# Kernel tuning notes

Measured on AMD Instinct MI355X. Metric: run time of the kernel, lower is better.

Reference implementation:

```python
import jax, jax.numpy as jnp
import numpy as np

EPS = 1e-5
NUM_HEADS = 8


def setup_inputs() -> dict:
    key = jax.random.key(0)
    ks = jax.random.split(key, 6)
    B, C, S = 4, 512, 2048
    std = 0.02
    return {
        "hidden_states": jax.random.normal(ks[0], (B, C, S), dtype=jnp.float32),
        "gn_weight": jnp.ones((C,), dtype=jnp.float32),
        "gn_bias": jnp.zeros((C,), dtype=jnp.float32),
        "wq": jax.random.normal(ks[1], (C, C), dtype=jnp.float32) * std,
        "bq": jnp.zeros((C,), dtype=jnp.float32),
        "wk": jax.random.normal(ks[2], (C, C), dtype=jnp.float32) * std,
        "bk": jnp.zeros((C,), dtype=jnp.float32),
        "wv": jax.random.normal(ks[3], (C, C), dtype=jnp.float32) * std,
        "bv": jnp.zeros((C,), dtype=jnp.float32),
        "wo": jax.random.normal(ks[4], (C, C), dtype=jnp.float32) * std,
        "bo": jnp.zeros((C,), dtype=jnp.float32),
    }


def reference(hidden_states, gn_weight, gn_bias, wq, bq, wk, bk, wv, bv, wo, bo):
    # hidden_states: [B, C, S]
    x = hidden_states
    B, C, S = x.shape
    H = NUM_HEADS
    D = C // H

    # GroupNorm with 1 group: normalize over (C, S) per sample
    mean = jnp.mean(x, axis=(1, 2), keepdims=True)
    var = jnp.var(x, axis=(1, 2), keepdims=True)
    h = (x - mean) * jax.lax.rsqrt(var + EPS)
    h = h * gn_weight[None, :, None] + gn_bias[None, :, None]

    h = jnp.swapaxes(h, 1, 2)  # [B, S, C]

    q = h @ wq.T + bq  # [B, S, C]
    k = h @ wk.T + bk
    v = h @ wv.T + bv

    # split heads: [B, H, S, D]
    q = q.reshape(B, S, H, D).transpose(0, 2, 1, 3)
    k = k.reshape(B, S, H, D).transpose(0, 2, 1, 3)
    v = v.reshape(B, S, H, D).transpose(0, 2, 1, 3)

    scale = 1.0 / (D ** 0.25)  # applied to both q and k, as in source
    scores = jnp.einsum('bhqd,bhkd->bhqk', q * scale, k * scale)
    probs = jax.nn.softmax(scores, axis=-1)
    out = jnp.einsum('bhqk,bhkd->bhqd', probs, v)  # [B, H, S, D]

    out = out.transpose(0, 2, 1, 3).reshape(B, S, C)  # [B, S, C]
    out = out @ wo.T + bo
    out = jnp.swapaxes(out, 1, 2)  # [B, C, S]
    return out + hidden_states
```

## Files before the change

### kernel.cpp

```cpp
#include <hip/hip_runtime.h>

typedef __attribute__((ext_vector_type(8))) __bf16 bf16x8;
typedef __attribute__((ext_vector_type(4))) __bf16 bf16x4;
typedef __attribute__((ext_vector_type(4))) float f32x4;
typedef __attribute__((ext_vector_type(16))) float f32x16;

#define BSZ 4
#define CCH 512
#define SEQ 2048
#define NH  8
#define HD  64

__device__ __forceinline__ f32x4 mfma16(bf16x8 a, bf16x8 b, f32x4 c) {
  return __builtin_amdgcn_mfma_f32_16x16x32_bf16(a, b, c, 0, 0, 0);
}
__device__ __forceinline__ f32x16 mfma32(bf16x8 a, bf16x8 b, f32x16 c) {
  return __builtin_amdgcn_mfma_f32_32x32x16_bf16(a, b, c, 0, 0, 0);
}

__device__ __forceinline__ void gload16(const void* g, void* l) {
  __builtin_amdgcn_global_load_lds((const __attribute__((address_space(1))) void*)g,
                                   (__attribute__((address_space(3))) void*)l,
                                   16, 0, 0);
}

__device__ __forceinline__ unsigned cvtpk(float lo, float hi) {
  unsigned r;
  asm("v_cvt_pk_bf16_f32 %0, %1, %2" : "=v"(r) : "v"(lo), "v"(hi));
  return r;
}
__device__ __forceinline__ void pl32swap(unsigned& a, unsigned& b) {
  asm("v_permlane32_swap_b32 %0, %1" : "+v"(a), "+v"(b));
}

__global__ __launch_bounds__(256) void gn_partial(const float* __restrict__ x,
                                                  float* __restrict__ stats) {
  int b = blockIdx.y;
  const float4* xb = (const float4*)(x + ((size_t)b << 20) + (size_t)blockIdx.x * 16384);
  int tid = threadIdx.x;
  float s = 0.f, sq = 0.f;
#pragma unroll
  for (int i = 0; i < 16; ++i) {
    float4 v = xb[i * 256 + tid];
    s  += v.x + v.y + v.z + v.w;
    sq += v.x * v.x + v.y * v.y + v.z * v.z + v.w * v.w;
  }
#pragma unroll
  for (int o = 32; o > 0; o >>= 1) { s += __shfl_down(s, o); sq += __shfl_down(sq, o); }
  __shared__ float ls[4], lq[4];
  int w = tid >> 6;
  if ((tid & 63) == 0) { ls[w] = s; lq[w] = sq; }
  __syncthreads();
  if (tid == 0) {
    float S = ls[0] + ls[1] + ls[2] + ls[3];
    float Q = lq[0] + lq[1] + lq[2] + lq[3];
    atomicAdd(&stats[b], S);
    atomicAdd(&stats[4 + b], Q);
  }
}

__global__ void gn_final(float* stats) {
  int t = threadIdx.x;
  if (t < 4) {
    const float n = 1048576.f;
    float mean = stats[t] / n;
    float var = stats[4 + t] / n - mean * mean;
    stats[8 + t]  = mean;
    stats[12 + t] = rsqrtf(var + 1e-5f);
  }
}

__global__ __launch_bounds__(256) void norm_tr(const float* __restrict__ x,
                                               const float* __restrict__ gw,
                                               const float* __restrict__ gb,
                                               const float* __restrict__ stats,
                                               __bf16* __restrict__ h) {
  int s0 = blockIdx.x * 64, c0 = blockIdx.y * 64, b = blockIdx.z;
  float mean = stats[8 + b], rstd = stats[12 + b];
  const float* xb = x + ((size_t)b << 20);
  __shared__ __align__(16) __bf16 tile[64][72];
  int tid = threadIdx.x;
#pragma unroll
  for (int j = 0; j < 16; ++j) {
    int e = tid + j * 256;
    int cl = e >> 6, sl = e & 63;
    float vv = xb[(size_t)(c0 + cl) * 2048 + s0 + sl];
    float hn = (vv - mean) * rstd * gw[c0 + cl] + gb[c0 + cl];
    tile[cl][sl] = (__bf16)hn;
  }
  __syncthreads();
#pragma unroll
  for (int j = 0; j < 2; ++j) {
    int row = (tid >> 3) + j * 32;
    int cg = tid & 7;
    bf16x8 pk;
#pragma unroll
    for (int e = 0; e < 8; ++e) pk[e] = tile[cg * 8 + e][row];
    *(bf16x8*)&h[(size_t)((b << 11) + s0 + row) * 512 + c0 + cg * 8] = pk;
  }
}

__global__ __launch_bounds__(256) void wcvt(const float* __restrict__ wq, const float* __restrict__ wk,
                                            const float* __restrict__ wv, const float* __restrict__ wo,
                                            __bf16* __restrict__ out) {
  int i = blockIdx.x * 256 + threadIdx.x;
  out[i]          = (__bf16)wq[i];
  out[262144 + i] = (__bf16)wk[i];
  out[524288 + i] = (__bf16)wv[i];
  out[786432 + i] = (__bf16)wo[i];
}

__global__ __launch_bounds__(256) void gemm_qkv(const __bf16* __restrict__ A, const __bf16* __restrict__ Wb,
                                                const float* __restrict__ bq, const float* __restrict__ bk,
                                                const float* __restrict__ bvv,
                                                __bf16* __restrict__ oq, __bf16* __restrict__ ok,
                                                __bf16* __restrict__ ov) {
  __shared__ __align__(16) __bf16 As[128 * 64];
  __shared__ __align__(16) __bf16 Bs[128 * 64];
  int z = blockIdx.z;
  const __bf16* W = Wb + (size_t)z * 262144;
  const float* bias = z == 0 ? bq : (z == 1 ? bk : bvv);
  __bf16* out = z == 0 ? oq : (z == 1 ? ok : ov);
  int tid = threadIdx.x, wid = tid >> 6, l = tid & 63;
  int m0 = blockIdx.x * 128, n0 = blockIdx.y * 128;
  int wm = (wid >> 1) * 64, wn = (wid & 1) * 64;
  int l16 = l & 15, lg = l >> 4;
  f32x4 zero = {0.f, 0.f, 0.f, 0.f};
  f32x4 acc[4][4];
#pragma unroll
  for (int mt = 0; mt < 4; ++mt)
#pragma unroll
    for (int nt = 0; nt < 4; ++nt) acc[mt][nt] = zero;
  int srow = wid * 32 + (l >> 3);
  int scol = (l & 7) * 8;
  for (int k0 = 0; k0 < 512; k0 += 64) {
    __syncthreads();
#pragma unroll
    for (int t = 0; t < 4; ++t) {
      gload16(A + (size_t)(m0 + srow + t * 8) * 512 + k0 + scol, &As[(wid * 32 + t * 8) * 64]);
      gload16(W + (size_t)(n0 + srow + t * 8) * 512 + k0 + scol, &Bs[(wid * 32 + t * 8) * 64]);
    }
    __syncthreads();
#pragma unroll
    for (int kk = 0; kk < 64; kk += 32) {
      bf16x8 af[4], bfr[4];
#pragma unroll
      for (int mt = 0; mt < 4; ++mt) af[mt] = *(const bf16x8*)&As[(wm + mt * 16 + l16) * 64 + kk + lg * 8];
#pragma unroll
      for (int nt = 0; nt < 4; ++nt) bfr[nt] = *(const bf16x8*)&Bs[(wn + nt * 16 + l16) * 64 + kk + lg * 8];
#pragma unroll
      for (int mt = 0; mt < 4; ++mt)
#pragma unroll
        for (int nt = 0; nt < 4; ++nt) acc[mt][nt] = mfma16(af[mt], bfr[nt], acc[mt][nt]);
    }
  }
#pragma unroll
  for (int nt = 0; nt < 4; ++nt) {
    int col = n0 + wn + nt * 16 + l16;
    float bb = bias[col];
#pragma unroll
    for (int mt = 0; mt < 4; ++mt)
#pragma unroll
      for (int r = 0; r < 4; ++r)
        out[(size_t)(m0 + wm + mt * 16 + lg * 4 + r) * 512 + col] = (__bf16)(acc[mt][nt][r] + bb);
  }
}

__global__ __launch_bounds__(256) void v_tr(const __bf16* __restrict__ v, __bf16* __restrict__ vt) {
  int s0 = blockIdx.x * 64, hh = blockIdx.y, b = blockIdx.z;
  __shared__ __align__(16) __bf16 tile[64][72];
  int tid = threadIdx.x;
#pragma unroll
  for (int j = 0; j < 16; ++j) {
    int e = tid + j * 256;
    int sl = e >> 6, dl = e & 63;
    tile[dl][sl] = v[(size_t)((b << 11) + s0 + sl) * 512 + hh * 64 + dl];
  }
  __syncthreads();
  const size_t base = (size_t)((b * 8 + hh) * 64) * 2048;
#pragma unroll
  for (int j = 0; j < 2; ++j) {
    int d = tid >> 2;
    int ch = (tid & 3) + j * 4;
    bf16x8 pk = *(const bf16x8*)&tile[d][ch * 8];
    *(bf16x8*)&vt[base + (size_t)d * 2048 + s0 + ch * 8] = pk;
  }
}

__global__ __launch_bounds__(256) void attn(const __bf16* __restrict__ q, const __bf16* __restrict__ k,
                                            const __bf16* __restrict__ vt, __bf16* __restrict__ ao) {
  const float C2 = 0.18033688011f;
  const float THR = 8.0f;
  int tid = threadIdx.x, w = tid >> 6, l = tid & 63;
  int q0w = blockIdx.x * 128 + w * 32;
  int hh = blockIdx.y, b = blockIdx.z;
  int l31 = l & 31, hi = l >> 5;

  __shared__ __align__(16) __bf16 smem[2][8192];

  bf16x8 qf[4];
  {
    const __bf16* qrow = q + ((size_t)((b << 11) + q0w + l31)) * 512 + hh * 64 + hi * 8;
#pragma unroll
    for (int dt = 0; dt < 4; ++dt) qf[dt] = *(const bf16x8*)&qrow[dt * 16];
  }

  const __bf16* kbase = k + ((size_t)(b << 11)) * 512 + hh * 64;
  const __bf16* vtb = vt + ((size_t)((b * 8 + hh) * 64)) * 2048;

  f32x16 zero16 = {};
  f32x16 o2[2];
  o2[0] = zero16; o2[1] = zero16;
  float m_run = -3.0e38f, l_run = 0.f;

  int rloc = l >> 3;
  int slotg = (l & 7) ^ rloc;
  int swz = (l31 & 7);

  auto STAGE = [&](int buf, int kv0) {
#pragma unroll
    for (int i = 0; i < 4; ++i) {
      int c = w * 4 + i;
      int row = (c & 7) * 8 + rloc;
      if (c < 8) {
        gload16(kbase + (size_t)(kv0 + row) * 512 + slotg * 8, &smem[buf][c * 512]);
      } else {
        gload16(vtb + (size_t)row * 2048 + kv0 + slotg * 8, &smem[buf][4096 + (c - 8) * 512]);
      }
    }
  };

  auto COMPUTE = [&](int buf) {
    const __bf16* Kt = &smem[buf][0];
    const __bf16* Vts = &smem[buf][4096];
    f32x16 sc[2];
#pragma unroll
    for (int kb = 0; kb < 2; ++kb) {
      sc[kb] = zero16;
      int r = kb * 32 + l31;
      __builtin_amdgcn_s_setprio(1);
#pragma unroll
      for (int dt = 0; dt < 4; ++dt) {
        bf16x8 kf = *(const bf16x8*)&Kt[r * 64 + ((dt * 2 + hi) ^ swz) * 8];
        sc[kb] = mfma32(kf, qf[dt], sc[kb]);
      }
      __builtin_amdgcn_s_setprio(0);
    }

    float mx01 = -3.0e38f;
#pragma unroll
    for (int kb = 0; kb < 2; ++kb)
#pragma unroll
      for (int r = 0; r < 16; ++r) mx01 = fmaxf(mx01, sc[kb][r]);
    mx01 = fmaxf(mx01, __shfl_xor(mx01, 32));
    mx01 *= C2;
    if (!__all(mx01 <= m_run + THR)) {
      float mnew = fmaxf(m_run, mx01);
      float alpha = exp2f(m_run - mnew);
      m_run = mnew;
      l_run *= alpha;
#pragma unroll
      for (int dblk = 0; dblk < 2; ++dblk)
#pragma unroll
        for (int r = 0; r < 16; ++r) o2[dblk][r] *= alpha;
    }
    float rs = 0.f;
#pragma unroll
    for (int kb = 0; kb < 2; ++kb)
#pragma unroll
      for (int r = 0; r < 16; ++r) {
        float p = exp2f(__builtin_fmaf(sc[kb][r], C2, -m_run));
        rs += p;
        sc[kb][r] = p;
      }
    rs += __shfl_xor(rs, 32);
    l_run += rs;

#pragma unroll
    for (int t = 0; t < 4; ++t) {
      int kb = t >> 1, h8 = (t & 1) * 8;
      unsigned u0 = cvtpk(sc[kb][h8 + 0], sc[kb][h8 + 1]);
      unsigned u1 = cvtpk(sc[kb][h8 + 2], sc[kb][h8 + 3]);
      unsigned u2 = cvtpk(sc[kb][h8 + 4], sc[kb][h8 + 5]);
      unsigned u3 = cvtpk(sc[kb][h8 + 6], sc[kb][h8 + 7]);
      pl32swap(u0, u2);
      pl32swap(u1, u3);
      union { unsigned u[4]; bf16x8 v; } pb;
      pb.u[0] = u0; pb.u[1] = u1; pb.u[2] = u2; pb.u[3] = u3;
      __builtin_amdgcn_s_setprio(1);
#pragma unroll
      for (int dblk = 0; dblk < 2; ++dblk) {
        int r = dblk * 32 + l31;
        bf16x8 vf = *(const bf16x8*)&Vts[r * 64 + ((t * 2 + hi) ^ swz) * 8];
        o2[dblk] = mfma32(vf, pb.v, o2[dblk]);
      }
      __builtin_amdgcn_s_setprio(0);
    }
  };

  int cur = 0;
  STAGE(0, 0);
  __syncthreads();
  for (int t = 0; t < 32; ++t) {
    if (t + 1 < 32) STAGE(cur ^ 1, (t + 1) * 64);
    COMPUTE(cur);
    __syncthreads();
    cur ^= 1;
  }

  float invl = 1.0f / l_run;
  __bf16* T = &smem[0][w * 2048];
  int swzq = (l31 & 7) * 8;
#pragma unroll
  for (int dblk = 0; dblk < 2; ++dblk)
#pragma unroll
    for (int g = 0; g < 4; ++g) {
      unsigned w0 = cvtpk(o2[dblk][g * 4 + 0] * invl, o2[dblk][g * 4 + 1] * invl);
      unsigned w1 = cvtpk(o2[dblk][g * 4 + 2] * invl, o2[dblk][g * 4 + 3] * invl);
      int d4 = dblk * 32 + g * 8 + hi * 4;
      uint2 pk2; pk2.x = w0; pk2.y = w1;
      *(uint2*)&T[l31 * 64 + (d4 ^ swzq)] = pk2;
    }
  int qr = l >> 1, hf = l & 1;
  int swzr = (qr & 7) * 8;
  __bf16* aorow = ao + (size_t)((b << 11) + q0w + qr) * 512 + hh * 64;
#pragma unroll
  for (int m = 0; m < 2; ++m) {
    int e = hf * 32 + m * 16;
    bf16x8 v0 = *(const bf16x8*)&T[qr * 64 + ((e) ^ swzr)];
    bf16x8 v1 = *(const bf16x8*)&T[qr * 64 + ((e + 8) ^ swzr)];
    *(bf16x8*)&aorow[e] = v0;
    *(bf16x8*)&aorow[e + 8] = v1;
  }
}

__global__ __launch_bounds__(256) void gemm_proj(const __bf16* __restrict__ A, const __bf16* __restrict__ W,
                                                 const float* __restrict__ bias,
                                                 const float* __restrict__ resid,
                                                 float* __restrict__ outp) {
  __shared__ __align__(16) union UU {
    struct SS { __bf16 a[128 * 64]; __bf16 b[128 * 64]; } s;
    float st[128 * 129];
  } u;
  int tid = threadIdx.x, wid = tid >> 6, l = tid & 63;
  int m0 = blockIdx.x * 128, n0 = blockIdx.y * 128;
  int wm = (wid >> 1) * 64, wn = (wid & 1) * 64;
  int l16 = l & 15, lg = l >> 4;
  f32x4 zero = {0.f, 0.f, 0.f, 0.f};
  f32x4 acc[4][4];
#pragma unroll
  for (int mt = 0; mt < 4; ++mt)
#pragma unroll
    for (int nt = 0; nt < 4; ++nt) acc[mt][nt] = zero;
  int srow = wid * 32 + (l >> 3);
  int scol = (l & 7) * 8;
  for (int k0 = 0; k0 < 512; k0 += 64) {
    __syncthreads();
#pragma unroll
    for (int t = 0; t < 4; ++t) {
      gload16(A + (size_t)(m0 + srow + t * 8) * 512 + k0 + scol, &u.s.a[(wid * 32 + t * 8) * 64]);
      gload16(W + (size_t)(n0 + srow + t * 8) * 512 + k0 + scol, &u.s.b[(wid * 32 + t * 8) * 64]);
    }
    __syncthreads();
#pragma unroll
    for (int kk = 0; kk < 64; kk += 32) {
      bf16x8 af[4], bfr[4];
#pragma unroll
      for (int mt = 0; mt < 4; ++mt) af[mt] = *(const bf16x8*)&u.s.a[(wm + mt * 16 + l16) * 64 + kk + lg * 8];
#pragma unroll
      for (int nt = 0; nt < 4; ++nt) bfr[nt] = *(const bf16x8*)&u.s.b[(wn + nt * 16 + l16) * 64 + kk + lg * 8];
#pragma unroll
      for (int mt = 0; mt < 4; ++mt)
#pragma unroll
        for (int nt = 0; nt < 4; ++nt) acc[mt][nt] = mfma16(af[mt], bfr[nt], acc[mt][nt]);
    }
  }
  __syncthreads();
#pragma unroll
  for (int nt = 0; nt < 4; ++nt) {
    int col = wn + nt * 16 + l16;
    float bb = bias[n0 + col];
#pragma unroll
    for (int mt = 0; mt < 4; ++mt)
#pragma unroll
      for (int r = 0; r < 4; ++r)
        u.st[(wm + mt * 16 + lg * 4 + r) * 129 + col] = acc[mt][nt][r] + bb;
  }
  __syncthreads();
  int b = m0 >> 11;
  int sbase = m0 & 2047;
  const float* rb = resid + ((size_t)b << 20);
  float* ob = outp + ((size_t)b << 20);
#pragma unroll
  for (int it = 0; it < 16; ++it) {
    int c = (tid >> 5) + it * 8;
    int s4 = (tid & 31) * 4;
    float4 r4 = *(const float4*)&rb[(size_t)(n0 + c) * 2048 + sbase + s4];
    float4 o4;
    o4.x = u.st[(s4 + 0) * 129 + c] + r4.x;
    o4.y = u.st[(s4 + 1) * 129 + c] + r4.y;
    o4.z = u.st[(s4 + 2) * 129 + c] + r4.z;
    o4.w = u.st[(s4 + 3) * 129 + c] + r4.w;
    *(float4*)&ob[(size_t)(n0 + c) * 2048 + sbase + s4] = o4;
  }
}

extern "C" void kernel_launch(void* const* d_in, const int* in_sizes, int n_in,
                              void* d_out, int out_size, void* d_ws, size_t ws_size,
                              hipStream_t stream) {
  const float* x   = (const float*)d_in[0];
  const float* gw  = (const float*)d_in[1];
  const float* gb  = (const float*)d_in[2];
  const float* wqf = (const float*)d_in[3];
  const float* bqf = (const float*)d_in[4];
  const float* wkf = (const float*)d_in[5];
  const float* bkf = (const float*)d_in[6];
  const float* wvf = (const float*)d_in[7];
  const float* bvf = (const float*)d_in[8];
  const float* wof = (const float*)d_in[9];
  const float* bof = (const float*)d_in[10];
  float* outp = (float*)d_out;

  char* ws = (char*)d_ws;
  float* stats = (float*)ws;
  const size_t MAT = (size_t)8192 * 512;
  __bf16* h  = (__bf16*)(ws + 256);
  __bf16* q  = h + MAT;
  __bf16* k  = q + MAT;
  __bf16* v  = k + MAT;
  __bf16* vt = v + MAT;
  __bf16* ao = vt + MAT;
  __bf16* wB = ao + MAT;

  hipMemsetAsync(stats, 0, 256, stream);
  gn_partial<<<dim3(64, 4), 256, 0, stream>>>(x, stats);
  gn_final<<<1, 64, 0, stream>>>(stats);
  norm_tr<<<dim3(32, 8, 4), 256, 0, stream>>>(x, gw, gb, stats, h);
  wcvt<<<1024, 256, 0, stream>>>(wqf, wkf, wvf, wof, wB);
  gemm_qkv<<<dim3(64, 4, 3), 256, 0, stream>>>(h, wB, bqf, bkf, bvf, q, k, v);
  v_tr<<<dim3(32, 8, 4), 256, 0, stream>>>(v, vt);
  attn<<<dim3(16, 8, 4), 256, 0, stream>>>(q, k, vt, ao);
  gemm_proj<<<dim3(64, 4), 256, 0, stream>>>(ao, wB + 3 * 262144, bof, x, outp);
}
```

Measured before the change: 225.3 us.

## Triple-buffer GEMM and attention loads, fuse V transpose into QKV epilogue

Both GEMMs move from a synchronous double-sync loop with 64-wide K tiles to a three-stage ring of 32-wide K tiles. The tiles use an XOR-swizzled LDS layout, a vmcnt-based wait plus a single barrier per step, and raised priority around the MFMA block. The attention kernel likewise moves to a three-buffer LDS ring with a two-tile lookahead. The V projection now writes directly in transposed [b,h,d,s] layout from the GEMM epilogue, removing the separate v_tr kernel and its intermediate buffer. In exchange there is more LDS per block, which may reduce occupancy, and the transposed V stores are narrow 8-byte writes scattered across rows.

```diff
diff --git a/kernel.cpp b/kernel.cpp
--- a/kernel.cpp
+++ b/kernel.cpp
@@ -32,6 +32,11 @@
 __device__ __forceinline__ void pl32swap(unsigned& a, unsigned& b) {
   asm("v_permlane32_swap_b32 %0, %1" : "+v"(a), "+v"(b));
 }
+
+#define WAIT_VM(N)                                          \
+  asm volatile("s_waitcnt vmcnt(" #N ")" ::: "memory");     \
+  __builtin_amdgcn_sched_barrier(0);                        \
+  __builtin_amdgcn_s_barrier();
 
 __global__ __launch_bounds__(256) void gn_partial(const float* __restrict__ x,
                                                   float* __restrict__ stats) {
@@ -114,13 +119,12 @@
                                                 const float* __restrict__ bq, const float* __restrict__ bk,
                                                 const float* __restrict__ bvv,
                                                 __bf16* __restrict__ oq, __bf16* __restrict__ ok,
-                                                __bf16* __restrict__ ov) {
-  __shared__ __align__(16) __bf16 As[128 * 64];
-  __shared__ __align__(16) __bf16 Bs[128 * 64];
+                                                __bf16* __restrict__ ovt) {
+  __shared__ __align__(16) __bf16 sA[3][4096];
+  __shared__ __align__(16) __bf16 sB[3][4096];
   int z = blockIdx.z;
   const __bf16* W = Wb + (size_t)z * 262144;
   const float* bias = z == 0 ? bq : (z == 1 ? bk : bvv);
-  __bf16* out = z == 0 ? oq : (z == 1 ? ok : ov);
   int tid = threadIdx.x, wid = tid >> 6, l = tid & 63;
   int m0 = blockIdx.x * 128, n0 = blockIdx.y * 128;
   int wm = (wid >> 1) * 64, wn = (wid & 1) * 64;
@@ -131,59 +135,70 @@
   for (int mt = 0; mt < 4; ++mt)
 #pragma unroll
     for (int nt = 0; nt < 4; ++nt) acc[mt][nt] = zero;
-  int srow = wid * 32 + (l >> 3);
-  int scol = (l & 7) * 8;
-  for (int k0 = 0; k0 < 512; k0 += 64) {
-    __syncthreads();
-#pragma unroll
-    for (int t = 0; t < 4; ++t) {
-      gload16(A + (size_t)(m0 + srow + t * 8) * 512 + k0 + scol, &As[(wid * 32 + t * 8) * 64]);
-      gload16(W + (size_t)(n0 + srow + t * 8) * 512 + k0 + scol, &Bs[(wid * 32 + t * 8) * 64]);
-    }
-    __syncthreads();
-#pragma unroll
-    for (int kk = 0; kk < 64; kk += 32) {
-      bf16x8 af[4], bfr[4];
-#pragma unroll
-      for (int mt = 0; mt < 4; ++mt) af[mt] = *(const bf16x8*)&As[(wm + mt * 16 + l16) * 64 + kk + lg * 8];
-#pragma unroll
-      for (int nt = 0; nt < 4; ++nt) bfr[nt] = *(const bf16x8*)&Bs[(wn + nt * 16 + l16) * 64 + kk + lg * 8];
+
+  int srow = wid * 32 + (l >> 2);
+  int scol = ((l & 3) ^ ((l >> 3) & 3)) * 8;
+  int rs = (lg ^ ((l16 >> 1) & 3)) * 8;
+
+  auto STG = [&](int buf, int k0) {
+#pragma unroll
+    for (int t = 0; t < 2; ++t) {
+      gload16(A + (size_t)(m0 + srow + t * 16) * 512 + k0 + scol, &sA[buf][(wid * 32 + t * 16) * 32]);
+      gload16(W + (size_t)(n0 + srow + t * 16) * 512 + k0 + scol, &sB[buf][(wid * 32 + t * 16) * 32]);
+    }
+  };
+  auto CMP = [&](int buf) {
+    bf16x8 af[4], bfr[4];
+#pragma unroll
+    for (int mt = 0; mt < 4; ++mt) af[mt] = *(const bf16x8*)&sA[buf][(wm + mt * 16 + l16) * 32 + rs];
+#pragma unroll
+    for (int nt = 0; nt < 4; ++nt) bfr[nt] = *(const bf16x8*)&sB[buf][(wn + nt * 16 + l16) * 32 + rs];
+    __builtin_amdgcn_s_setprio(1);
+#pragma unroll
+    for (int mt = 0; mt < 4; ++mt)
+#pragma unroll
+      for (int nt = 0; nt < 4; ++nt) acc[mt][nt] = mfma16(af[mt], bfr[nt], acc[mt][nt]);
+    __builtin_amdgcn_s_setprio(0);
+  };
+
+  STG(0, 0); STG(1, 32);
+  int bc = 0, sb = 2;
+  for (int t = 0; t < 15; ++t) {
+    WAIT_VM(4);
+    if (t < 14) { STG(sb, (t + 2) * 32); sb = sb == 2 ? 0 : sb + 1; }
+    CMP(bc); bc = bc == 2 ? 0 : bc + 1;
+  }
+  WAIT_VM(0);
+  CMP(bc);
+
+  if (z < 2) {
+    __bf16* out = z == 0 ? oq : ok;
+#pragma unroll
+    for (int nt = 0; nt < 4; ++nt) {
+      int col = n0 + wn + nt * 16 + l16;
+      float bb = bias[col];
 #pragma unroll
       for (int mt = 0; mt < 4; ++mt)
 #pragma unroll
-        for (int nt = 0; nt < 4; ++nt) acc[mt][nt] = mfma16(af[mt], bfr[nt], acc[mt][nt]);
-    }
-  }
-#pragma unroll
-  for (int nt = 0; nt < 4; ++nt) {
-    int col = n0 + wn + nt * 16 + l16;
-    float bb = bias[col];
-#pragma unroll
-    for (int mt = 0; mt < 4; ++mt)
-#pragma unroll
-      for (int r = 0; r < 4; ++r)
-        out[(size_t)(m0 + wm + mt * 16 + lg * 4 + r) * 512 + col] = (__bf16)(acc[mt][nt][r] + bb);
-  }
-}
-
-__global__ __launch_bounds__(256) void v_tr(const __bf16* __restrict__ v, __bf16* __restrict__ vt) {
-  int s0 = blockIdx.x * 64, hh = blockIdx.y, b = blockIdx.z;
-  __shared__ __align__(16) __bf16 tile[64][72];
-  int tid = threadIdx.x;
-#pragma unroll
-  for (int j = 0; j < 16; ++j) {
-    int e = tid + j * 256;
-    int sl = e >> 6, dl = e & 63;
-    tile[dl][sl] = v[(size_t)((b << 11) + s0 + sl) * 512 + hh * 64 + dl];
-  }
-  __syncthreads();
-  const size_t base = (size_t)((b * 8 + hh) * 64) * 2048;
-#pragma unroll
-  for (int j = 0; j < 2; ++j) {
-    int d = tid >> 2;
-    int ch = (tid & 3) + j * 4;
-    bf16x8 pk = *(const bf16x8*)&tile[d][ch * 8];
-    *(bf16x8*)&vt[base + (size_t)d * 2048 + s0 + ch * 8] = pk;
+        for (int r = 0; r < 4; ++r)
+          out[(size_t)(m0 + wm + mt * 16 + lg * 4 + r) * 512 + col] = (__bf16)(acc[mt][nt][r] + bb);
+    }
+  } else {
+#pragma unroll
+    for (int nt = 0; nt < 4; ++nt) {
+      int col = n0 + wn + nt * 16 + l16;
+      float bb = bias[col];
+      int hd = col >> 6, dd = col & 63;
+#pragma unroll
+      for (int mt = 0; mt < 4; ++mt) {
+        int sg = m0 + wm + mt * 16 + lg * 4;
+        int bI = sg >> 11, sl = sg & 2047;
+        bf16x4 pk;
+#pragma unroll
+        for (int r = 0; r < 4; ++r) pk[r] = (__bf16)(acc[mt][nt][r] + bb);
+        *(bf16x4*)&ovt[((size_t)((bI * 8 + hd) * 64 + dd)) * 2048 + sl] = pk;
+      }
+    }
   }
 }
 
@@ -196,7 +211,7 @@
   int hh = blockIdx.y, b = blockIdx.z;
   int l31 = l & 31, hi = l >> 5;
 
-  __shared__ __align__(16) __bf16 smem[2][8192];
+  __shared__ __align__(16) __bf16 smem[3][8192];
 
   bf16x8 qf[4];
   {
@@ -264,17 +279,17 @@
 #pragma unroll
         for (int r = 0; r < 16; ++r) o2[dblk][r] *= alpha;
     }
-    float rs = 0.f;
+    float rsum = 0.f;
 #pragma unroll
     for (int kb = 0; kb < 2; ++kb)
 #pragma unroll
       for (int r = 0; r < 16; ++r) {
         float p = exp2f(__builtin_fmaf(sc[kb][r], C2, -m_run));
-        rs += p;
+        rsum += p;
         sc[kb][r] = p;
       }
-    rs += __shfl_xor(rs, 32);
-    l_run += rs;
+    rsum += __shfl_xor(rsum, 32);
+    l_run += rsum;
 
 #pragma unroll
     for (int t = 0; t < 4; ++t) {
@@ -298,15 +313,16 @@
     }
   };
 
-  int cur = 0;
   STAGE(0, 0);
-  __syncthreads();
-  for (int t = 0; t < 32; ++t) {
-    if (t + 1 < 32) STAGE(cur ^ 1, (t + 1) * 64);
-    COMPUTE(cur);
-    __syncthreads();
-    cur ^= 1;
-  }
+  STAGE(1, 64);
+  int bc = 0, sb = 2;
+  for (int t = 0; t < 31; ++t) {
+    WAIT_VM(4);
+    if (t < 30) { STAGE(sb, (t + 2) * 64); sb = sb == 2 ? 0 : sb + 1; }
+    COMPUTE(bc); bc = bc == 2 ? 0 : bc + 1;
+  }
+  WAIT_VM(0);
+  COMPUTE(bc);
 
   float invl = 1.0f / l_run;
   __bf16* T = &smem[0][w * 2048];
@@ -339,7 +355,7 @@
                                                  const float* __restrict__ resid,
                                                  float* __restrict__ outp) {
   __shared__ __align__(16) union UU {
-    struct SS { __bf16 a[128 * 64]; __bf16 b[128 * 64]; } s;
+    struct SS { __bf16 a[3][4096]; __bf16 b[3][4096]; } s;
     float st[128 * 129];
   } u;
   int tid = threadIdx.x, wid = tid >> 6, l = tid & 63;
@@ -352,29 +368,42 @@
   for (int mt = 0; mt < 4; ++mt)
 #pragma unroll
     for (int nt = 0; nt < 4; ++nt) acc[mt][nt] = zero;
-  int srow = wid * 32 + (l >> 3);
-  int scol = (l & 7) * 8;
-  for (int k0 = 0; k0 < 512; k0 += 64) {
-    __syncthreads();
-#pragma unroll
-    for (int t = 0; t < 4; ++t) {
-      gload16(A + (size_t)(m0 + srow + t * 8) * 512 + k0 + scol, &u.s.a[(wid * 32 + t * 8) * 64]);
-      gload16(W + (size_t)(n0 + srow + t * 8) * 512 + k0 + scol, &u.s.b[(wid * 32 + t * 8) * 64]);
-    }
-    __syncthreads();
-#pragma unroll
-    for (int kk = 0; kk < 64; kk += 32) {
-      bf16x8 af[4], bfr[4];
-#pragma unroll
-      for (int mt = 0; mt < 4; ++mt) af[mt] = *(const bf16x8*)&u.s.a[(wm + mt * 16 + l16) * 64 + kk + lg * 8];
-#pragma unroll
-      for (int nt = 0; nt < 4; ++nt) bfr[nt] = *(const bf16x8*)&u.s.b[(wn + nt * 16 + l16) * 64 + kk + lg * 8];
-#pragma unroll
-      for (int mt = 0; mt < 4; ++mt)
-#pragma unroll
-        for (int nt = 0; nt < 4; ++nt) acc[mt][nt] = mfma16(af[mt], bfr[nt], acc[mt][nt]);
-    }
-  }
+
+  int srow = wid * 32 + (l >> 2);
+  int scol = ((l & 3) ^ ((l >> 3) & 3)) * 8;
+  int rs = (lg ^ ((l16 >> 1) & 3)) * 8;
+
+  auto STG = [&](int buf, int k0) {
+#pragma unroll
+    for (int t = 0; t < 2; ++t) {
+      gload16(A + (size_t)(m0 + srow + t * 16) * 512 + k0 + scol, &u.s.a[buf][(wid * 32 + t * 16) * 32]);
+      gload16(W + (size_t)(n0 + srow + t * 16) * 512 + k0 + scol, &u.s.b[buf][(wid * 32 + t * 16) * 32]);
+    }
+  };
+  auto CMP = [&](int buf) {
+    bf16x8 af[4], bfr[4];
+#pragma unroll
+    for (int mt = 0; mt < 4; ++mt) af[mt] = *(const bf16x8*)&u.s.a[buf][(wm + mt * 16 + l16) * 32 + rs];
+#pragma unroll
+    for (int nt = 0; nt < 4; ++nt) bfr[nt] = *(const bf16x8*)&u.s.b[buf][(wn + nt * 16 + l16) * 32 + rs];
+    __builtin_amdgcn_s_setprio(1);
+#pragma unroll
+    for (int mt = 0; mt < 4; ++mt)
+#pragma unroll
+      for (int nt = 0; nt < 4; ++nt) acc[mt][nt] = mfma16(af[mt], bfr[nt], acc[mt][nt]);
+    __builtin_amdgcn_s_setprio(0);
+  };
+
+  STG(0, 0); STG(1, 32);
+  int bc = 0, sb = 2;
+  for (int t = 0; t < 15; ++t) {
+    WAIT_VM(4);
+    if (t < 14) { STG(sb, (t + 2) * 32); sb = sb == 2 ? 0 : sb + 1; }
+    CMP(bc); bc = bc == 2 ? 0 : bc + 1;
+  }
+  WAIT_VM(0);
+  CMP(bc);
+
   __syncthreads();
 #pragma unroll
   for (int nt = 0; nt < 4; ++nt) {
@@ -427,8 +456,7 @@
   __bf16* h  = (__bf16*)(ws + 256);
   __bf16* q  = h + MAT;
   __bf16* k  = q + MAT;
-  __bf16* v  = k + MAT;
-  __bf16* vt = v + MAT;
+  __bf16* vt = k + MAT;
   __bf16* ao = vt + MAT;
   __bf16* wB = ao + MAT;
 
@@ -437,8 +465,7 @@
   gn_final<<<1, 64, 0, stream>>>(stats);
   norm_tr<<<dim3(32, 8, 4), 256, 0, stream>>>(x, gw, gb, stats, h);
   wcvt<<<1024, 256, 0, stream>>>(wqf, wkf, wvf, wof, wB);
-  gemm_qkv<<<dim3(64, 4, 3), 256, 0, stream>>>(h, wB, bqf, bkf, bvf, q, k, v);
-  v_tr<<<dim3(32, 8, 4), 256, 0, stream>>>(v, vt);
+  gemm_qkv<<<dim3(64, 4, 3), 256, 0, stream>>>(h, wB, bqf, bkf, bvf, q, k, vt);
   attn<<<dim3(16, 8, 4), 256, 0, stream>>>(q, k, vt, ao);
   gemm_proj<<<dim3(64, 4), 256, 0, stream>>>(ao, wB + 3 * 262144, bof, x, outp);
 }
```

Result: faster. 208.2 us (-7.6%).
